# Optimization experiments

Hardware: AMD Instinct MI355X
Metric: run time of the kernel (lower is better)

The kernel has to match this reference:

```python
import jax, jax.numpy as jnp
import numpy as np

N_TOK, EMBED, N_CLS, BATCH, N_HEAD = 32768, 512, 16, 8, 8
D_HEAD = EMBED // N_HEAD


def setup_inputs() -> dict:
    key0 = jax.random.key(0)
    ks = jax.random.split(key0, 12)
    s = 1.0 / np.sqrt(EMBED)
    query = jax.random.normal(ks[0], (N_TOK, EMBED), dtype=jnp.float32)
    key_f = jax.random.normal(ks[1], (N_CLS, BATCH, EMBED), dtype=jnp.float32)
    val_f = jax.random.normal(ks[2], (N_CLS, BATCH, EMBED), dtype=jnp.float32)
    batch_idx = jnp.sort(jax.random.randint(ks[3], (N_TOK,), 0, BATCH)).astype(jnp.int32)
    Wq = jax.random.normal(ks[4], (EMBED, EMBED), dtype=jnp.float32) * s
    bq = jnp.zeros((EMBED,), dtype=jnp.float32)
    Wk = jax.random.normal(ks[5], (EMBED, EMBED), dtype=jnp.float32) * s  # Conv1d(k=1) kernel squeezed
    bk = jnp.zeros((EMBED,), dtype=jnp.float32)
    Wv = jax.random.normal(ks[6], (EMBED, EMBED), dtype=jnp.float32) * s
    bv = jnp.zeros((EMBED,), dtype=jnp.float32)
    Wo = jax.random.normal(ks[7], (EMBED, EMBED), dtype=jnp.float32) * s
    bo = jnp.zeros((EMBED,), dtype=jnp.float32)
    return {"query": query, "key": key_f, "value": val_f, "batch_idx": batch_idx,
            "batch_size": BATCH, "Wq": Wq, "bq": bq, "Wk": Wk, "bk": bk,
            "Wv": Wv, "bv": bv, "Wo": Wo, "bo": bo}


def reference(query, key, value, batch_idx, batch_size, Wq, bq, Wk, bk, Wv, bv, Wo, bo):
    n_tok, embed = query.shape
    L, B, _ = key.shape
    H, D = N_HEAD, EMBED // N_HEAD
    scale = D ** -0.5  # matmul_norm
    # projections (Conv1d with kernel_size=1 == pointwise linear over E)
    q = (query @ Wq.T + bq).reshape(n_tok, H, D)                           # [N,H,D]
    k = (jnp.einsum('lbe,fe->blf', key, Wk) + bk)                          # [B,L,E]
    k = k.transpose(0, 2, 1).reshape(B, H, D, L)                           # [B,H,D,L]
    v = (jnp.einsum('lbe,fe->blf', value, Wv) + bv)                        # [B,L,E]
    v = v.transpose(0, 2, 1).reshape(B, H, D, L).transpose(0, 1, 3, 2)     # [B,H,L,D]
    # scores against every batch's prototypes, then pick each token's batch
    scores_all = jnp.einsum('nhd,bhdl->nbhl', q, k) * scale                # [N,B,H,L]
    sel = batch_idx.astype(jnp.int32)[:, None, None, None]
    scores = jnp.take_along_axis(scores_all, sel, axis=1).squeeze(1)       # [N,H,L]
    p = jax.nn.softmax(scores, axis=-1)
    ctx_all = jnp.einsum('nhl,bhld->nbhd', p, v)                           # [N,B,H,D]
    ctx = jnp.take_along_axis(ctx_all, sel, axis=1).squeeze(1)             # [N,H,D]
    return ctx.reshape(n_tok, embed) @ Wo.T + bo
```

## Files before the change

### kernel.cpp

```cpp
#include <hip/hip_runtime.h>

typedef unsigned short u16;
typedef __attribute__((ext_vector_type(8))) short short8;
typedef __attribute__((ext_vector_type(4))) unsigned short u16x4;
typedef __attribute__((ext_vector_type(4))) float f32x4;

#define N_TOKENS 32768
#define EMBED 512
#define NCLS 16
#define NBATCH 8
#define NHEAD 8
#define DHEAD 64

__device__ __forceinline__ u16 f2bf(float f) {
  unsigned u = __float_as_uint(f);
  u += 0x7fffu + ((u >> 16) & 1u);
  return (u16)(u >> 16);
}

__device__ __forceinline__ void async16(const u16* g, u16* l) {
  __builtin_amdgcn_global_load_lds(
      (__attribute__((address_space(1))) const unsigned int*)(const void*)g,
      (__attribute__((address_space(3))) unsigned int*)(void*)l,
      16, 0, 0);
}

__global__ __launch_bounds__(256) void kvproj_kernel(
    const float* __restrict__ key, const float* __restrict__ val,
    const float* __restrict__ Wk, const float* __restrict__ bk,
    const float* __restrict__ Wv, const float* __restrict__ bv,
    float* __restrict__ kproj, float* __restrict__ vproj) {
  const int blk = blockIdx.x;
  const bool isV = blk & 1;
  const int b = (blk >> 1) & 7;
  const int l = (blk >> 4) & 15;
  const int fg = blk >> 8;
  const int wave = threadIdx.x >> 6;
  const int lane = threadIdx.x & 63;
  const int fbase = fg * 64 + wave * 16;
  const float* x = (isV ? val : key) + ((size_t)l * NBATCH + b) * EMBED;
  const float* W = isV ? Wv : Wk;
  const float* bias = isV ? bv : bk;

  float4 x0 = *(const float4*)(x + lane * 8);
  float4 x1 = *(const float4*)(x + lane * 8 + 4);

#pragma unroll
  for (int grp = 0; grp < 4; grp++) {
    float acc[4];
#pragma unroll
    for (int j = 0; j < 4; j++) {
      const float* w = W + (size_t)(fbase + grp * 4 + j) * EMBED + lane * 8;
      float4 w0 = *(const float4*)w;
      float4 w1 = *(const float4*)(w + 4);
      acc[j] = x0.x * w0.x + x0.y * w0.y + x0.z * w0.z + x0.w * w0.w +
               x1.x * w1.x + x1.y * w1.y + x1.z * w1.z + x1.w * w1.w;
    }
#pragma unroll
    for (int j = 0; j < 4; j++) {
      acc[j] += __shfl_xor(acc[j], 1);
      acc[j] += __shfl_xor(acc[j], 2);
      acc[j] += __shfl_xor(acc[j], 4);
      acc[j] += __shfl_xor(acc[j], 8);
      acc[j] += __shfl_xor(acc[j], 16);
      acc[j] += __shfl_xor(acc[j], 32);
    }
#pragma unroll
    for (int j = 0; j < 4; j++) {
      if (lane == j) {
        const int f = fbase + grp * 4 + j;
        float v = acc[j] + bias[f];
        if (!isV) {
          kproj[((size_t)(b * EMBED + f)) * NCLS + l] = v;
        } else {
          vproj[(size_t)b * 8192 + (size_t)(f >> 6) * 1024 + l * 64 + (f & 63)] = v;
        }
      }
    }
  }
}

__global__ __launch_bounds__(256) void build_all(
    const float* __restrict__ kproj, const float* __restrict__ vproj,
    const float* __restrict__ Wq, const float* __restrict__ bq,
    const float* __restrict__ Wo,
    u16* __restrict__ Kqb, u16* __restrict__ WoVb, float* __restrict__ sb) {
  const int blk = blockIdx.x;
  if (blk < 2048) {
    int t = blk * 256 + threadIdx.x;
    int e = t & 511;
    int hl = (t >> 9) & 127;
    int b = t >> 16;
    int h = hl >> 4, l = hl & 15;
    const float* kp = kproj + (size_t)b * 8192 + h * 1024 + l;
    const float* wq = Wq + (size_t)(h * 64) * 512 + e;
    float acc = 0.f;
#pragma unroll 16
    for (int d = 0; d < 64; d++) acc += kp[d * 16] * wq[d * 512];
    Kqb[t] = f2bf(acc);
  } else if (blk < 3072) {
    const int wave = threadIdx.x >> 6;
    const int lane = threadIdx.x & 63;
    const int wgid = (blk - 2048) * 4 + wave;
    const int b = wgid >> 9, f = wgid & 511;
    const int l = lane >> 2, c = lane & 3;
    const float* vp = vproj + (size_t)b * 8192 + l * 64 + c * 16;
    const float* wo = Wo + (size_t)f * 512 + c * 16;
#pragma unroll 2
    for (int h = 0; h < 8; h++) {
      const float* v = vp + h * 1024;
      const float* w = wo + h * 64;
      float4 v0 = *(const float4*)v,       w0 = *(const float4*)w;
      float4 v1 = *(const float4*)(v + 4), w1 = *(const float4*)(w + 4);
      float4 v2 = *(const float4*)(v + 8), w2 = *(const float4*)(w + 8);
      float4 v3 = *(const float4*)(v + 12), w3 = *(const float4*)(w + 12);
      float acc = v0.x * w0.x + v0.y * w0.y + v0.z * w0.z + v0.w * w0.w +
                  v1.x * w1.x + v1.y * w1.y + v1.z * w1.z + v1.w * w1.w +
                  v2.x * w2.x + v2.y * w2.y + v2.z * w2.z + v2.w * w2.w +
                  v3.x * w3.x + v3.y * w3.y + v3.z * w3.z + v3.w * w3.w;
      acc += __shfl_xor(acc, 1);
      acc += __shfl_xor(acc, 2);
      if (c == 0) WoVb[(size_t)b * 65536 + (size_t)f * 128 + h * 16 + l] = f2bf(acc);
    }
  } else {
    int t = (blk - 3072) * 256 + threadIdx.x;
    int hl = t & 127, b = t >> 7;
    int h = hl >> 4, l = hl & 15;
    const float* kp = kproj + (size_t)b * 8192 + h * 1024 + l;
    const float* q = bq + h * 64;
    float acc = 0.f;
#pragma unroll
    for (int d = 0; d < 64; d++) acc += q[d] * kp[d * 16];
    sb[t] = acc;
  }
}

__global__ __launch_bounds__(256) void fused_attn(
    const float* __restrict__ query, const u16* __restrict__ Kqb,
    const u16* __restrict__ WoVb, const float* __restrict__ sb,
    const float* __restrict__ bo, const int* __restrict__ bidx,
    float* __restrict__ out) {
  __shared__ __align__(16) u16 Bs[2][128 * 32];
  __shared__ __align__(16) u16 Ps[64 * 128];
  const int tid = threadIdx.x;
  const int lane = tid & 63;
  const int wave = tid >> 6;
  const int quad = lane >> 4;
  const int l16 = lane & 15;
  const int tileId = blockIdx.x & 511;
  const int slot = blockIdx.x >> 9;
  const int m0 = tileId * 64;
  const int bFirst = bidx[m0];
  const int bLast = bidx[m0 + 63];
  if (slot == 1 && bFirst == bLast) return;
  const int b0 = (slot == 0) ? bFirst : bFirst + 1;
  const int b1 = (slot == 0) ? bFirst : bLast;

  const int r0 = tid >> 2, r1 = r0 + 64;
  const int lg0 = (tid & 3) ^ ((r0 >> 1) & 3);
  const int lg1 = (tid & 3) ^ ((r1 >> 1) & 3);
  const size_t boff0 = (size_t)r0 * 512 + lg0 * 8;
  const size_t boff1 = (size_t)r1 * 512 + lg1 * 8;

  const float* pA = query + (size_t)(m0 + wave * 16 + l16) * 512 + quad * 8;
  short8 aReg[16];
#pragma unroll
  for (int t = 0; t < 16; t++) {
    float4 a0 = *(const float4*)(pA + t * 32);
    float4 a1 = *(const float4*)(pA + t * 32 + 4);
    short8 v;
    v[0] = (short)f2bf(a0.x); v[1] = (short)f2bf(a0.y);
    v[2] = (short)f2bf(a0.z); v[3] = (short)f2bf(a0.w);
    v[4] = (short)f2bf(a1.x); v[5] = (short)f2bf(a1.y);
    v[6] = (short)f2bf(a1.z); v[7] = (short)f2bf(a1.w);
    aReg[t] = v;
  }

  for (int bb = b0; bb <= b1; bb++) {
    const u16* Bq = Kqb + (size_t)bb * 65536;

    async16(Bq + boff0, &Bs[0][tid * 8]);
    async16(Bq + boff1, &Bs[0][tid * 8 + 2048]);

    f32x4 acc1[8];
#pragma unroll
    for (int j = 0; j < 8; j++) acc1[j] = (f32x4){0.f, 0.f, 0.f, 0.f};

#pragma unroll
    for (int t = 0; t < 16; t++) {
      __syncthreads();
      const int cur = t & 1;
      if (t < 15) {
        const int ko = (t + 1) * 32;
        async16(Bq + boff0 + ko, &Bs[cur ^ 1][tid * 8]);
        async16(Bq + boff1 + ko, &Bs[cur ^ 1][tid * 8 + 2048]);
      }
      __builtin_amdgcn_s_setprio(1);
#pragma unroll
      for (int ni = 0; ni < 8; ni++) {
        const int rw = ni * 16 + l16;
        short8 bfr = *(const short8*)&Bs[cur][rw * 32 + ((quad ^ ((rw >> 1) & 3)) << 3)];
        acc1[ni] = __builtin_amdgcn_mfma_f32_16x16x32_bf16(aReg[t], bfr, acc1[ni], 0, 0, 0);
      }
      __builtin_amdgcn_s_setprio(0);
    }

    float sbv[8];
#pragma unroll
    for (int ni = 0; ni < 8; ni++) sbv[ni] = sb[bb * 128 + ni * 16 + l16];
#pragma unroll
    for (int r = 0; r < 4; r++) {
      const int row = wave * 16 + quad * 4 + r;
#pragma unroll
      for (int ni = 0; ni < 8; ni++) {
        float v = acc1[ni][r] + sbv[ni];
        float mx = v;
        mx = fmaxf(mx, __shfl_xor(mx, 1));
        mx = fmaxf(mx, __shfl_xor(mx, 2));
        mx = fmaxf(mx, __shfl_xor(mx, 4));
        mx = fmaxf(mx, __shfl_xor(mx, 8));
        float ev = __expf((v - mx) * 0.125f);
        float s = ev;
        s += __shfl_xor(s, 1);
        s += __shfl_xor(s, 2);
        s += __shfl_xor(s, 4);
        s += __shfl_xor(s, 8);
        const int col = ni * 16 + l16;
        Ps[row * 128 + (((col >> 3) ^ (row & 7)) << 3) + (col & 7)] = f2bf(ev / s);
      }
    }
    __syncthreads();

    const u16* Wv = WoVb + (size_t)bb * 65536;
#pragma unroll
    for (int h2 = 0; h2 < 2; h2++) {
      const int f0 = wave * 128 + h2 * 64;
      f32x4 acc2[4][4];
#pragma unroll
      for (int i = 0; i < 4; i++)
#pragma unroll
        for (int j = 0; j < 4; j++) acc2[i][j] = (f32x4){0.f, 0.f, 0.f, 0.f};
#pragma unroll
      for (int kk = 0; kk < 4; kk++) {
        short8 paf[4], bf2[4];
#pragma unroll
        for (int mi = 0; mi < 4; mi++) {
          const int row = mi * 16 + l16;
          paf[mi] = *(const short8*)&Ps[row * 128 + (((kk * 4 + quad) ^ (row & 7)) << 3)];
        }
#pragma unroll
        for (int ni = 0; ni < 4; ni++) {
          const int fr = f0 + ni * 16 + l16;
          bf2[ni] = *(const short8*)(Wv + (size_t)fr * 128 + kk * 32 + quad * 8);
        }
        __builtin_amdgcn_s_setprio(1);
#pragma unroll
        for (int mi = 0; mi < 4; mi++)
#pragma unroll
          for (int ni = 0; ni < 4; ni++)
            acc2[mi][ni] = __builtin_amdgcn_mfma_f32_16x16x32_bf16(paf[mi], bf2[ni], acc2[mi][ni], 0, 0, 0);
        __builtin_amdgcn_s_setprio(0);
      }
      float bov[4];
#pragma unroll
      for (int ni = 0; ni < 4; ni++) bov[ni] = bo[f0 + ni * 16 + l16];
#pragma unroll
      for (int mi = 0; mi < 4; mi++)
#pragma unroll
        for (int r = 0; r < 4; r++) {
          const int rb = bidx[m0 + mi * 16 + quad * 4 + r];
          if (rb == bb) {
            const size_t row = m0 + mi * 16 + quad * 4 + r;
#pragma unroll
            for (int ni = 0; ni < 4; ni++)
              out[row * 512 + f0 + ni * 16 + l16] = acc2[mi][ni][r] + bov[ni];
          }
        }
    }
    __syncthreads();
  }
}

extern "C" void kernel_launch(void* const* d_in, const int* in_sizes, int n_in,
                              void* d_out, int out_size, void* d_ws, size_t ws_size,
                              hipStream_t stream) {
  const float* query = (const float*)d_in[0];
  const float* keyt = (const float*)d_in[1];
  const float* valt = (const float*)d_in[2];
  const int* bidx = (const int*)d_in[3];
  const float* Wq = (const float*)d_in[5];
  const float* bq = (const float*)d_in[6];
  const float* Wk = (const float*)d_in[7];
  const float* bk = (const float*)d_in[8];
  const float* Wv = (const float*)d_in[9];
  const float* bv = (const float*)d_in[10];
  const float* Wo = (const float*)d_in[11];
  const float* bo = (const float*)d_in[12];
  float* out = (float*)d_out;

  unsigned char* w = (unsigned char*)d_ws;
  float* kproj = (float*)(w + 41943040ull);
  float* vproj = (float*)(w + 42205184ull);
  u16* Kqb = (u16*)(w + 42467328ull);
  u16* WoVb = (u16*)(w + 43515904ull);
  float* sb = (float*)(w + 44564480ull);

  kvproj_kernel<<<2048, 256, 0, stream>>>(keyt, valt, Wk, bk, Wv, bv, kproj, vproj);

  build_all<<<3076, 256, 0, stream>>>(kproj, vproj, Wq, bq, Wo, Kqb, WoVb, sb);

  fused_attn<<<N_TOKENS / 64 * 2, 256, 0, stream>>>(query, Kqb, WoVb, sb, bo, bidx, out);
}
```

Baseline: 228.1 us.

## Stream query fragments per k-step instead of holding all in registers; remap tiles

Replaces the 16-entry bf16 query register cache with a one-step-ahead prefetch of fp32 query data inside the K loop, converting each step on the fly, and stops fully unrolling that loop. The goal is lower register pressure and higher occupancy. In exchange, query rows are re-read and re-converted for every batch slot a tile spans. The change also permutes the block-to-tile mapping, interleaving tiles across the grid, and caches per-row batch indices in registers instead of reloading them in the epilogue.

```diff
diff --git a/kernel.cpp b/kernel.cpp
--- a/kernel.cpp
+++ b/kernel.cpp
@@ -147,8 +147,9 @@
   const int wave = tid >> 6;
   const int quad = lane >> 4;
   const int l16 = lane & 15;
-  const int tileId = blockIdx.x & 511;
+  const int raw = blockIdx.x & 511;
   const int slot = blockIdx.x >> 9;
+  const int tileId = ((raw & 7) << 6) | (raw >> 3);
   const int m0 = tileId * 64;
   const int bFirst = bidx[m0];
   const int bLast = bidx[m0 + 63];
@@ -162,31 +163,26 @@
   const size_t boff0 = (size_t)r0 * 512 + lg0 * 8;
   const size_t boff1 = (size_t)r1 * 512 + lg1 * 8;
 
+  int rowb[4][4];
+#pragma unroll
+  for (int mi = 0; mi < 4; mi++)
+#pragma unroll
+    for (int r = 0; r < 4; r++) rowb[mi][r] = bidx[m0 + mi * 16 + quad * 4 + r];
+
   const float* pA = query + (size_t)(m0 + wave * 16 + l16) * 512 + quad * 8;
-  short8 aReg[16];
-#pragma unroll
-  for (int t = 0; t < 16; t++) {
-    float4 a0 = *(const float4*)(pA + t * 32);
-    float4 a1 = *(const float4*)(pA + t * 32 + 4);
-    short8 v;
-    v[0] = (short)f2bf(a0.x); v[1] = (short)f2bf(a0.y);
-    v[2] = (short)f2bf(a0.z); v[3] = (short)f2bf(a0.w);
-    v[4] = (short)f2bf(a1.x); v[5] = (short)f2bf(a1.y);
-    v[6] = (short)f2bf(a1.z); v[7] = (short)f2bf(a1.w);
-    aReg[t] = v;
-  }
 
   for (int bb = b0; bb <= b1; bb++) {
     const u16* Bq = Kqb + (size_t)bb * 65536;
 
     async16(Bq + boff0, &Bs[0][tid * 8]);
     async16(Bq + boff1, &Bs[0][tid * 8 + 2048]);
+    float4 a0c = *(const float4*)(pA);
+    float4 a1c = *(const float4*)(pA + 4);
 
     f32x4 acc1[8];
 #pragma unroll
     for (int j = 0; j < 8; j++) acc1[j] = (f32x4){0.f, 0.f, 0.f, 0.f};
 
-#pragma unroll
     for (int t = 0; t < 16; t++) {
       __syncthreads();
       const int cur = t & 1;
@@ -195,12 +191,22 @@
         async16(Bq + boff0 + ko, &Bs[cur ^ 1][tid * 8]);
         async16(Bq + boff1 + ko, &Bs[cur ^ 1][tid * 8 + 2048]);
       }
+      float4 a0 = a0c, a1 = a1c;
+      if (t < 15) {
+        a0c = *(const float4*)(pA + (t + 1) * 32);
+        a1c = *(const float4*)(pA + (t + 1) * 32 + 4);
+      }
+      short8 af;
+      af[0] = (short)f2bf(a0.x); af[1] = (short)f2bf(a0.y);
+      af[2] = (short)f2bf(a0.z); af[3] = (short)f2bf(a0.w);
+      af[4] = (short)f2bf(a1.x); af[5] = (short)f2bf(a1.y);
+      af[6] = (short)f2bf(a1.z); af[7] = (short)f2bf(a1.w);
       __builtin_amdgcn_s_setprio(1);
 #pragma unroll
       for (int ni = 0; ni < 8; ni++) {
         const int rw = ni * 16 + l16;
         short8 bfr = *(const short8*)&Bs[cur][rw * 32 + ((quad ^ ((rw >> 1) & 3)) << 3)];
-        acc1[ni] = __builtin_amdgcn_mfma_f32_16x16x32_bf16(aReg[t], bfr, acc1[ni], 0, 0, 0);
+        acc1[ni] = __builtin_amdgcn_mfma_f32_16x16x32_bf16(af, bfr, acc1[ni], 0, 0, 0);
       }
       __builtin_amdgcn_s_setprio(0);
     }
@@ -268,8 +274,7 @@
       for (int mi = 0; mi < 4; mi++)
 #pragma unroll
         for (int r = 0; r < 4; r++) {
-          const int rb = bidx[m0 + mi * 16 + quad * 4 + r];
-          if (rb == bb) {
+          if (rowb[mi][r] == bb) {
             const size_t row = m0 + mi * 16 + quad * 4 + r;
 #pragma unroll
             for (int ni = 0; ni < 4; ni++)
```

New measurement: 242.0 us. +6.1%, slower.
